# Optimization experiments

Measured on AMD Instinct MI355X. Metric: run time of the kernel, lower is better.

## Reference

```python
import jax, jax.numpy as jnp
import numpy as np

EPS = 1e-5
MAX_DIFF = 0.01


def _conv1d(x, w, b, pad):
    # x: [B,C,L], w: [O,I,K]
    out = jax.lax.conv_general_dilated(x, w, (1,), [(pad, pad)],
                                       dimension_numbers=('NCH', 'OIH', 'NCH'))
    return out + b[None, :, None]


def _maxpool2(x):
    B, C, L = x.shape
    return x.reshape(B, C, L // 2, 2).max(-1)


def setup_inputs() -> dict:
    key = jax.random.key(0)
    ks = jax.random.split(key, 12)
    B, N, F, NF = 64, 750, 8, 250
    inp = {
        'x_sample': jax.random.normal(ks[0], (B, NF), jnp.float32),
        'x_graph': jax.random.normal(ks[1], (B, N, F), jnp.float32),
        'W1': jax.random.normal(ks[2], (NF, 250), jnp.float32) * 0.05,
        'b1': jnp.zeros((250,), jnp.float32),
        'gl': jnp.ones((250,), jnp.float32),
        'bl': jnp.zeros((250,), jnp.float32),
        'Wg': jax.random.normal(ks[3], (F, F), jnp.float32) * 0.3,
        'bg': jnp.zeros((F,), jnp.float32),
        'g1': jnp.ones((1,), jnp.float32),
        'be1': jnp.zeros((1,), jnp.float32),
        'Wc1': jax.random.normal(ks[4], (32, 1, 5), jnp.float32) * 0.3,
        'bc1': jnp.zeros((32,), jnp.float32),
        'gc1': jnp.ones((32,), jnp.float32),
        'bec1': jnp.zeros((32,), jnp.float32),
        'Wc2': jax.random.normal(ks[5], (64, 32, 5), jnp.float32) * 0.08,
        'bc2': jnp.zeros((64,), jnp.float32),
        'gc2': jnp.ones((64,), jnp.float32),
        'bec2': jnp.zeros((64,), jnp.float32),
        'Wc3': jax.random.normal(ks[6], (128, 64, 250), jnp.float32) * 0.008,
        'bc3': jnp.zeros((128,), jnp.float32),
        'Wf': jax.random.normal(ks[7], (128, 64), jnp.float32) * 0.09,
        'bf': jnp.zeros((64,), jnp.float32),
        'gf': jnp.ones((64,), jnp.float32),
        'bef': jnp.zeros((64,), jnp.float32),
        'Wo': jax.random.normal(ks[8], (64, 12), jnp.float32) * 0.12,
        'bo': jnp.zeros((12,), jnp.float32),
    }
    return inp


def reference(x_sample, x_graph, W1, b1, gl, bl, Wg, bg, g1, be1,
              Wc1, bc1, gc1, bec1, Wc2, bc2, gc2, bec2, Wc3, bc3,
              Wf, bf, gf, bef, Wo, bo):
    inv = 1.0 / jnp.sqrt(1.0 + EPS)  # eval-mode BN with mean=0, var=1
    B, N, F = x_graph.shape

    # linear1 -> BN -> ReLU (dropout is identity in eval)
    s = x_sample @ W1 + b1
    s = jax.nn.relu(s * inv * gl + bl)  # [B,250]

    # pairwise-threshold edge construction as dense masked adjacency
    d = x_graph[..., 0]  # [B,N]
    mask = (d[:, :, None] - d[:, None, :]) ** 2 < MAX_DIFF  # symmetric
    eye = jnp.eye(N, dtype=x_graph.dtype)
    A = jnp.where(mask, 1.0, 0.0) * (1.0 - eye) + eye  # + self loops (GCNConv)
    dn = jax.lax.rsqrt(A.sum(-1))  # D^{-1/2}
    An = dn[:, :, None] * A * dn[:, None, :]

    # GCNConv: D^{-1/2}(A+I)D^{-1/2} (X W) + b
    h = jnp.einsum('bij,bjf->bif', An, x_graph @ Wg) + bg
    # BatchNorm2d(1) eval (scalar affine) -> ReLU
    h = jax.nn.relu(h * inv * g1[0] + be1[0])  # [B,N,F]

    g = h.mean(-1)  # [B,N]
    x = jnp.concatenate([s, g], axis=1)[:, None, :]  # [B,1,1000]

    x = _conv1d(x, Wc1, bc1, pad=2)
    x = jax.nn.relu(x * inv * gc1[None, :, None] + bec1[None, :, None])
    x = _maxpool2(x)  # [B,32,500]

    x = _conv1d(x, Wc2, bc2, pad=2)
    x = jax.nn.relu(x * inv * gc2[None, :, None] + bec2[None, :, None])
    x = _maxpool2(x)  # [B,64,250]

    x = _conv1d(x, Wc3, bc3, pad=0)[:, :, 0]  # [B,128]

    x = x @ Wf + bf
    x = jax.nn.relu(x * inv * gf + bef)
    x = x @ Wo + bo
    return jax.nn.log_softmax(x, axis=1)
```

## Files before the change

### kernel.cpp

```cpp
#include <hip/hip_runtime.h>
#include <math.h>

#define NN 750

__device__ __forceinline__ float bn_inv() { return 1.0f / sqrtf(1.0f + 1e-5f); }

__device__ __forceinline__ unsigned encf(float f) {
  unsigned b = __float_as_uint(f);
  return (b & 0x80000000u) ? ~b : (b | 0x80000000u);
}
__device__ __forceinline__ float decf(unsigned u) {
  return __uint_as_float((u & 0x80000000u) ? (u & 0x7fffffffu) : ~u);
}

__global__ __launch_bounds__(256) void k_lin1(
    const float* __restrict__ xs, const float* __restrict__ W1,
    const float* __restrict__ b1, const float* __restrict__ gl,
    const float* __restrict__ bl, float* __restrict__ X0)
{
  int b = blockIdx.x, t = threadIdx.x;
  __shared__ float xsh[250];
  for (int k = t; k < 250; k += 256) xsh[k] = xs[b * 250 + k];
  __syncthreads();
  if (t < 250) {
    float acc = 0.f;
    #pragma unroll 10
    for (int k = 0; k < 250; ++k) acc = fmaf(xsh[k], W1[k * 250 + t], acc);
    float v = (acc + b1[t]) * bn_inv() * gl[t] + bl[t];
    X0[b * 1000 + t] = fmaxf(v, 0.f);
  }
}

__global__ __launch_bounds__(256) void k_gcn_count(
    const float* __restrict__ xg, const float* __restrict__ Wg,
    float* __restrict__ szdn, int* __restrict__ loA, int* __restrict__ hiA,
    float* __restrict__ dnA)
{
  int b = blockIdx.x, c = blockIdx.y, t = threadIdx.x;
  __shared__ unsigned long long kL[NN];
  __shared__ float wgs[64];
  for (int j = t; j < NN; j += 256) {
    float dj = xg[(size_t)(b * NN + j) * 8];
    kL[j] = ((unsigned long long)encf(dj) << 10) | (unsigned)j;
  }
  if (t < 64) wgs[t] = Wg[t];
  __syncthreads();
  if (t >= 250) return;
  int i = c * 250 + t;
  float d = xg[(size_t)(b * NN + i) * 8];
  unsigned long long ki = ((unsigned long long)encf(d) << 10) | (unsigned)i;

  unsigned uf = encf(d - 0.15f);
  unsigned ut = encf(d);
  #pragma unroll 1
  for (int it = 0; it < 33 && (ut - uf) > 1u; ++it) {
    unsigned um = uf + ((ut - uf) >> 1);
    if (d - decf(um) >= 0.1f) uf = um; else ut = um;
  }
  unsigned A1 = ut;
  unsigned vf = encf(d);
  unsigned vt = encf(d + 0.15f);
  #pragma unroll 1
  for (int it = 0; it < 33 && (vt - vf) > 1u; ++it) {
    unsigned um = vf + ((vt - vf) >> 1);
    if (d - decf(um) <= -0.1f) vt = um; else vf = um;
  }
  unsigned B = vt;

  unsigned long long KA = (unsigned long long)A1 << 10;
  unsigned long long KB = (unsigned long long)B << 10;
  int rank = 0, lov = 0, hiv = 0;
  #pragma unroll 6
  for (int j = 0; j < NN; ++j) {
    unsigned long long kj = kL[j];
    rank += (kj < ki);
    lov  += (kj < KA);
    hiv  += (kj < KB);
  }
  int cnt = hiv - lov;
  float dn = 1.0f / sqrtf((float)cnt);

  const float4* xp = (const float4*)(xg + (size_t)(b * NN + i) * 8);
  float4 x0 = xp[0], x1 = xp[1];
  float xv[8] = {x0.x, x0.y, x0.z, x0.w, x1.x, x1.y, x1.z, x1.w};
  float zf[8];
  #pragma unroll
  for (int f = 0; f < 8; ++f) {
    float a = 0.f;
    #pragma unroll
    for (int k = 0; k < 8; ++k) a = fmaf(xv[k], wgs[k * 8 + f], a);
    zf[f] = dn * a;
  }
  float* dst = szdn + ((size_t)b * NN + rank) * 8;
  *(float4*)dst       = make_float4(zf[0], zf[1], zf[2], zf[3]);
  *(float4*)(dst + 4) = make_float4(zf[4], zf[5], zf[6], zf[7]);
  loA[b * NN + i] = lov; hiA[b * NN + i] = hiv; dnA[b * NN + i] = dn;
}

__global__ __launch_bounds__(512) void k_gcn_apply(
    const float* __restrict__ szdn, const int* __restrict__ loA,
    const int* __restrict__ hiA, const float* __restrict__ dnA,
    const float* __restrict__ bgp, const float* __restrict__ g1p,
    const float* __restrict__ be1p, float* __restrict__ X0)
{
  int b = blockIdx.x, t = threadIdx.x;
  __shared__ float P[NN * 8];
  __shared__ float wsum[4 * 8];
  __shared__ float bgs[8];
  if (t < 8) bgs[t] = bgp[t];
  for (int e = t; e < NN * 2; e += 512)
    ((float4*)P)[e] = ((const float4*)(szdn + (size_t)b * NN * 8))[e];
  __syncthreads();

  int lane = t & 63, w = t >> 6;
  bool scanner = (t < 256);
  float e0[8], e01[8], s[8], sc[8];
  if (scanner) {
    int u = t;
    if (u < 250) {
      #pragma unroll
      for (int f = 0; f < 8; ++f) e0[f] = P[(3 * u) * 8 + f];
      #pragma unroll
      for (int f = 0; f < 8; ++f) e01[f] = e0[f] + P[(3 * u + 1) * 8 + f];
      #pragma unroll
      for (int f = 0; f < 8; ++f) s[f] = e01[f] + P[(3 * u + 2) * 8 + f];
    } else {
      #pragma unroll
      for (int f = 0; f < 8; ++f) { e0[f] = 0.f; e01[f] = 0.f; s[f] = 0.f; }
    }
    #pragma unroll
    for (int f = 0; f < 8; ++f) sc[f] = s[f];
    for (int dlt = 1; dlt < 64; dlt <<= 1) {
      float o[8];
      #pragma unroll
      for (int f = 0; f < 8; ++f) o[f] = __shfl_up(sc[f], (unsigned)dlt, 64);
      if (lane >= dlt) {
        #pragma unroll
        for (int f = 0; f < 8; ++f) sc[f] += o[f];
      }
    }
    if (lane == 63) {
      #pragma unroll
      for (int f = 0; f < 8; ++f) wsum[w * 8 + f] = sc[f];
    }
  }
  __syncthreads();
  if (scanner && t < 250) {
    float off[8];
    #pragma unroll
    for (int f = 0; f < 8; ++f) off[f] = 0.f;
    for (int ww = 0; ww < w; ++ww) {
      #pragma unroll
      for (int f = 0; f < 8; ++f) off[f] += wsum[ww * 8 + f];
    }
    int u = t;
    #pragma unroll
    for (int f = 0; f < 8; ++f) {
      float excl = sc[f] - s[f] + off[f];
      P[(3 * u) * 8 + f]     = excl + e0[f];
      P[(3 * u + 1) * 8 + f] = excl + e01[f];
      P[(3 * u + 2) * 8 + f] = excl + s[f];
    }
  }
  __syncthreads();

  float inv = bn_inv(), g1v = g1p[0], be1v = be1p[0];
  for (int nn = t; nn < NN; nn += 512) {
    int lo = loA[b * NN + nn], hi = hiA[b * NN + nn];
    float dn = dnA[b * NN + nn];
    float gsum = 0.f;
    #pragma unroll
    for (int f = 0; f < 8; ++f) {
      float a  = P[(hi - 1) * 8 + f];
      float bb = (lo > 0) ? P[(lo - 1) * 8 + f] : 0.f;
      float h  = dn * (a - bb) + bgs[f];
      float v  = h * inv * g1v + be1v;
      gsum += fmaxf(v, 0.f);
    }
    X0[b * 1000 + 250 + nn] = gsum * 0.125f;
  }
}

__global__ __launch_bounds__(256) void k_conv1(
    const float* __restrict__ X0, const float* __restrict__ Wc1,
    const float* __restrict__ bc1, const float* __restrict__ gc1,
    const float* __restrict__ bec1, float* __restrict__ Y1)
{
  int b = blockIdx.x, p0 = blockIdx.y * 125, tid = threadIdx.x;
  __shared__ float xsh[254];
  __shared__ float w[160], bb[32], gg[32], ee[32];
  for (int i = tid; i < 254; i += 256) {
    int gq = 2 * p0 - 2 + i;
    xsh[i] = (gq >= 0 && gq < 1000) ? X0[b * 1000 + gq] : 0.f;
  }
  for (int i = tid; i < 160; i += 256) w[i] = Wc1[i];
  if (tid < 32) { bb[tid] = bc1[tid]; gg[tid] = gc1[tid]; ee[tid] = bec1[tid]; }
  __syncthreads();
  float inv = bn_inv();
  for (int o = tid; o < 32 * 125; o += 256) {
    int c = o / 125, pl = o % 125;
    int base = 2 * pl;
    float v0 = 0.f, v1 = 0.f;
    #pragma unroll
    for (int k = 0; k < 5; ++k) {
      float wk = w[c * 5 + k];
      v0 = fmaf(xsh[base + k], wk, v0);
      v1 = fmaf(xsh[base + 1 + k], wk, v1);
    }
    float s0 = fmaxf((v0 + bb[c]) * inv * gg[c] + ee[c], 0.f);
    float s1 = fmaxf((v1 + bb[c]) * inv * gg[c] + ee[c], 0.f);
    Y1[((b * 32) + c) * 500 + p0 + pl] = fmaxf(s0, s1);
  }
}

__global__ __launch_bounds__(256) void k_conv2(
    const float* __restrict__ Y1, const float* __restrict__ Wc2,
    const float* __restrict__ bc2, const float* __restrict__ gc2,
    const float* __restrict__ bec2, float* __restrict__ Y2)
{
  int b = blockIdx.x, p0 = blockIdx.y * 52, tid = threadIdx.x;
  __shared__ float xin[32][108];
  __shared__ float ws2[64 * 161];
  for (int e = tid; e < 32 * 108; e += 256) {
    int ci = e / 108, li = e % 108;
    int gq = 2 * p0 - 2 + li;
    xin[ci][li] = (gq >= 0 && gq < 500) ? Y1[((b * 32) + ci) * 500 + gq] : 0.f;
  }
  for (int e = tid; e < 64 * 160; e += 256) {
    int co = e / 160, r = e % 160;
    ws2[co * 161 + r] = Wc2[e];
  }
  __syncthreads();
  int co = tid >> 2, sub = tid & 3;
  int base = sub * 26;
  float acc[26];
  #pragma unroll
  for (int r = 0; r < 26; ++r) acc[r] = 0.f;
  for (int ci = 0; ci < 32; ++ci) {
    float xr[30];
    #pragma unroll
    for (int jj = 0; jj < 30; ++jj) xr[jj] = xin[ci][base + jj];
    #pragma unroll
    for (int k = 0; k < 5; ++k) {
      float wk = ws2[co * 161 + ci * 5 + k];
      #pragma unroll
      for (int r = 0; r < 26; ++r) acc[r] = fmaf(xr[r + k], wk, acc[r]);
    }
  }
  float inv = bn_inv();
  float bc = bc2[co], gc = gc2[co], ec = bec2[co];
  int ps = p0 + sub * 13;
  #pragma unroll
  for (int r = 0; r < 13; ++r) {
    int p = ps + r;
    if (p < 250) {
      float a0 = fmaxf((acc[2 * r] + bc) * inv * gc + ec, 0.f);
      float a1 = fmaxf((acc[2 * r + 1] + bc) * inv * gc + ec, 0.f);
      Y2[((b * 64) + co) * 250 + p] = fmaxf(a0, a1);
    }
  }
}

__global__ __launch_bounds__(256) void k_conv3(
    const float* __restrict__ Y2, const float* __restrict__ Wc3,
    float* __restrict__ C3P, int CP)
{
  int pb = blockIdx.x, tid = threadIdx.x;
  __shared__ float As[64 * 64];
  __shared__ float Bs[64 * 128];
  int bt = tid >> 5, ot = tid & 31;
  int b0 = bt * 8, o0 = ot * 4;
  float4 acc[8];
  #pragma unroll
  for (int r = 0; r < 8; ++r) acc[r] = make_float4(0.f, 0.f, 0.f, 0.f);

  for (int s = 0; s < CP; ++s) {
    int kbase = (pb * CP + s) * 64;
    __syncthreads();
    for (int e = tid; e < 4096; e += 256) {
      int bb = e >> 6, kk = e & 63;
      As[e] = Y2[bb * 16000 + kbase + kk];
    }
    for (int e = tid; e < 8192; e += 256) {
      int o = e >> 6, kk = e & 63;
      float v = Wc3[o * 16000 + kbase + kk];
      Bs[kk * 128 + ((((o >> 2) ^ (kk & 31)) << 2) | (o & 3))] = v;
    }
    __syncthreads();
    for (int ks = 0; ks < 64; ks += 4) {
      float4 av[8];
      #pragma unroll
      for (int r = 0; r < 8; ++r)
        av[r] = *(const float4*)&As[(b0 + r) * 64 + ks];
      float4 bv[4];
      #pragma unroll
      for (int q = 0; q < 4; ++q) {
        int kk = ks + q;
        bv[q] = *(const float4*)&Bs[kk * 128 + ((ot ^ (kk & 31)) << 2)];
      }
      #pragma unroll
      for (int q = 0; q < 4; ++q) {
        #pragma unroll
        for (int r = 0; r < 8; ++r) {
          float a = (q == 0) ? av[r].x : (q == 1) ? av[r].y
                  : (q == 2) ? av[r].z : av[r].w;
          acc[r].x = fmaf(a, bv[q].x, acc[r].x);
          acc[r].y = fmaf(a, bv[q].y, acc[r].y);
          acc[r].z = fmaf(a, bv[q].z, acc[r].z);
          acc[r].w = fmaf(a, bv[q].w, acc[r].w);
        }
      }
    }
  }
  #pragma unroll
  for (int r = 0; r < 8; ++r)
    *(float4*)&C3P[(size_t)pb * 8192 + (b0 + r) * 128 + o0] = acc[r];
}

__global__ __launch_bounds__(256) void k_fc(
    const float* __restrict__ C3P, const float* __restrict__ bc3,
    const float* __restrict__ Wf, const float* __restrict__ bf,
    const float* __restrict__ gf, const float* __restrict__ bef,
    const float* __restrict__ Wo, const float* __restrict__ bo,
    float* __restrict__ out, int NB)
{
  int b = blockIdx.x, t = threadIdx.x;
  __shared__ float zp[8][128];
  __shared__ float z[128];
  __shared__ float fp[4][64];
  __shared__ float f[64];

  int g = t >> 5;
  int o4 = (t & 31) * 4;
  float4 a = make_float4(0.f, 0.f, 0.f, 0.f);
  for (int c = g; c < NB; c += 8) {
    float4 v = *(const float4*)&C3P[(size_t)c * 8192 + b * 128 + o4];
    a.x += v.x; a.y += v.y; a.z += v.z; a.w += v.w;
  }
  *(float4*)&zp[g][o4] = a;
  __syncthreads();
  if (t < 128) {
    float s = bc3[t];
    #pragma unroll
    for (int gg = 0; gg < 8; ++gg) s += zp[gg][t];
    z[t] = s;
  }
  __syncthreads();
  {
    int oo = t & 63, q = t >> 6;
    float acc = 0.f;
    #pragma unroll
    for (int k = 0; k < 32; ++k) {
      int kk = q * 32 + k;
      acc = fmaf(z[kk], Wf[kk * 64 + oo], acc);
    }
    fp[q][oo] = acc;
  }
  __syncthreads();
  if (t < 64) {
    float v = fp[0][t] + fp[1][t] + fp[2][t] + fp[3][t] + bf[t];
    v = v * bn_inv() * gf[t] + bef[t];
    f[t] = fmaxf(v, 0.f);
  }
  __syncthreads();

  if (t < 64) {
    float logit = 0.f;
    if (t < 12) {
      float acc = 0.f;
      #pragma unroll 8
      for (int k = 0; k < 64; ++k) acc = fmaf(f[k], Wo[k * 12 + t], acc);
      logit = acc + bo[t];
    }
    float m = (t < 12) ? logit : -3.4e38f;
    for (int off = 32; off > 0; off >>= 1) m = fmaxf(m, __shfl_xor(m, off));
    float e = (t < 12) ? expf(logit - m) : 0.f;
    float ssum = e;
    for (int off = 32; off > 0; off >>= 1) ssum += __shfl_xor(ssum, off);
    if (t < 12) out[b * 12 + t] = logit - m - logf(ssum);
  }
}

extern "C" void kernel_launch(void* const* d_in, const int* in_sizes, int n_in,
                              void* d_out, int out_size, void* d_ws, size_t ws_size,
                              hipStream_t stream)
{
  const float* xs   = (const float*)d_in[0];
  const float* xg   = (const float*)d_in[1];
  const float* W1   = (const float*)d_in[2];
  const float* b1   = (const float*)d_in[3];
  const float* gl   = (const float*)d_in[4];
  const float* bl   = (const float*)d_in[5];
  const float* Wg   = (const float*)d_in[6];
  const float* bg   = (const float*)d_in[7];
  const float* g1   = (const float*)d_in[8];
  const float* be1  = (const float*)d_in[9];
  const float* Wc1  = (const float*)d_in[10];
  const float* bc1  = (const float*)d_in[11];
  const float* gc1  = (const float*)d_in[12];
  const float* bec1 = (const float*)d_in[13];
  const float* Wc2  = (const float*)d_in[14];
  const float* bc2  = (const float*)d_in[15];
  const float* gc2  = (const float*)d_in[16];
  const float* bec2 = (const float*)d_in[17];
  const float* Wc3  = (const float*)d_in[18];
  const float* bc3  = (const float*)d_in[19];
  const float* Wf   = (const float*)d_in[20];
  const float* bfp  = (const float*)d_in[21];
  const float* gf   = (const float*)d_in[22];
  const float* bef  = (const float*)d_in[23];
  const float* Wo   = (const float*)d_in[24];
  const float* bo   = (const float*)d_in[25];
  float* out = (float*)d_out;

  float* W    = (float*)d_ws;
  float* X0   = W;
  float* Y1   = W + 64000;
  float* Y2   = W + 1088000;
  float* szdn = W + 2112000;
  int*   loA  = (int*)(W + 2496000);
  int*   hiA  = (int*)(W + 2544000);
  float* dnA  = W + 2592000;
  float* C3P  = W + 2640000;

  long availl = (long)(ws_size / 4) - 2640000L;
  const int cand[8] = {250, 125, 50, 25, 10, 5, 2, 1};
  int NB = 1;
  for (int i = 0; i < 8; ++i)
    if ((long)cand[i] * 8192L <= availl) { NB = cand[i]; break; }
  int CP = 250 / NB;

  k_lin1     <<<64, 256, 0, stream>>>(xs, W1, b1, gl, bl, X0);
  k_gcn_count<<<dim3(64, 3), 256, 0, stream>>>(xg, Wg, szdn, loA, hiA, dnA);
  k_gcn_apply<<<64, 512, 0, stream>>>(szdn, loA, hiA, dnA, bg, g1, be1, X0);
  k_conv1    <<<dim3(64, 4), 256, 0, stream>>>(X0, Wc1, bc1, gc1, bec1, Y1);
  k_conv2    <<<dim3(64, 5), 256, 0, stream>>>(Y1, Wc2, bc2, gc2, bec2, Y2);
  k_conv3    <<<NB, 256, 0, stream>>>(Y2, Wc3, C3P, CP);
  k_fc       <<<64, 256, 0, stream>>>(C3P, bc3, Wf, bfp, gf, bef, Wo, bo, out, NB);
}
```

Before: 200.4 us.

## Fuse lin1 into GCN count kernel and conv1 into GCN apply kernel

Result: faster. 194.3 us (-3.0%).

```diff
diff --git a/kernel.cpp b/kernel.cpp
--- a/kernel.cpp
+++ b/kernel.cpp
@@ -13,32 +13,32 @@
   return __uint_as_float((u & 0x80000000u) ? (u & 0x7fffffffu) : ~u);
 }
 
-__global__ __launch_bounds__(256) void k_lin1(
+__global__ __launch_bounds__(256) void k_front(
     const float* __restrict__ xs, const float* __restrict__ W1,
     const float* __restrict__ b1, const float* __restrict__ gl,
-    const float* __restrict__ bl, float* __restrict__ X0)
-{
-  int b = blockIdx.x, t = threadIdx.x;
-  __shared__ float xsh[250];
-  for (int k = t; k < 250; k += 256) xsh[k] = xs[b * 250 + k];
-  __syncthreads();
-  if (t < 250) {
-    float acc = 0.f;
-    #pragma unroll 10
-    for (int k = 0; k < 250; ++k) acc = fmaf(xsh[k], W1[k * 250 + t], acc);
-    float v = (acc + b1[t]) * bn_inv() * gl[t] + bl[t];
-    X0[b * 1000 + t] = fmaxf(v, 0.f);
-  }
-}
-
-__global__ __launch_bounds__(256) void k_gcn_count(
-    const float* __restrict__ xg, const float* __restrict__ Wg,
+    const float* __restrict__ bl, const float* __restrict__ xg,
+    const float* __restrict__ Wg, float* __restrict__ X0s,
     float* __restrict__ szdn, int* __restrict__ loA, int* __restrict__ hiA,
     float* __restrict__ dnA)
 {
-  int b = blockIdx.x, c = blockIdx.y, t = threadIdx.x;
+  int b = blockIdx.x, t = threadIdx.x;
   __shared__ unsigned long long kL[NN];
   __shared__ float wgs[64];
+  __shared__ float xsh[250];
+
+  if (blockIdx.y == 3) {
+    for (int k = t; k < 250; k += 256) xsh[k] = xs[b * 250 + k];
+    __syncthreads();
+    if (t < 250) {
+      float acc = 0.f;
+      #pragma unroll 10
+      for (int k = 0; k < 250; ++k) acc = fmaf(xsh[k], W1[k * 250 + t], acc);
+      float v = (acc + b1[t]) * bn_inv() * gl[t] + bl[t];
+      X0s[b * 250 + t] = fmaxf(v, 0.f);
+    }
+    return;
+  }
+  int c = blockIdx.y;
   for (int j = t; j < NN; j += 256) {
     float dj = xg[(size_t)(b * NN + j) * 8];
     kL[j] = ((unsigned long long)encf(dj) << 10) | (unsigned)j;
@@ -50,16 +50,14 @@
   float d = xg[(size_t)(b * NN + i) * 8];
   unsigned long long ki = ((unsigned long long)encf(d) << 10) | (unsigned)i;
 
-  unsigned uf = encf(d - 0.15f);
-  unsigned ut = encf(d);
+  unsigned uf = encf(d - 0.15f), ut = encf(d);
   #pragma unroll 1
   for (int it = 0; it < 33 && (ut - uf) > 1u; ++it) {
     unsigned um = uf + ((ut - uf) >> 1);
     if (d - decf(um) >= 0.1f) uf = um; else ut = um;
   }
   unsigned A1 = ut;
-  unsigned vf = encf(d);
-  unsigned vt = encf(d + 0.15f);
+  unsigned vf = encf(d), vt = encf(d + 0.15f);
   #pragma unroll 1
   for (int it = 0; it < 33 && (vt - vf) > 1u; ++it) {
     unsigned um = vf + ((vt - vf) >> 1);
@@ -97,17 +95,29 @@
   loA[b * NN + i] = lov; hiA[b * NN + i] = hiv; dnA[b * NN + i] = dn;
 }
 
-__global__ __launch_bounds__(512) void k_gcn_apply(
+__global__ __launch_bounds__(512) void k_apply1(
     const float* __restrict__ szdn, const int* __restrict__ loA,
     const int* __restrict__ hiA, const float* __restrict__ dnA,
     const float* __restrict__ bgp, const float* __restrict__ g1p,
-    const float* __restrict__ be1p, float* __restrict__ X0)
+    const float* __restrict__ be1p, const float* __restrict__ X0s,
+    const float* __restrict__ Wc1, const float* __restrict__ bc1,
+    const float* __restrict__ gc1, const float* __restrict__ bec1,
+    float* __restrict__ Y1)
 {
   int b = blockIdx.x, t = threadIdx.x;
   __shared__ float P[NN * 8];
   __shared__ float wsum[4 * 8];
   __shared__ float bgs[8];
+  __shared__ float xpad[1004];
+  __shared__ float w1s[160], bb1[32], gg1[32], ee1[32];
+
   if (t < 8) bgs[t] = bgp[t];
+  for (int i = t; i < 160; i += 512) w1s[i] = Wc1[i];
+  if (t >= 256 && t < 288) {
+    int q = t - 256; bb1[q] = bc1[q]; gg1[q] = gc1[q]; ee1[q] = bec1[q];
+  }
+  if (t >= 288 && t < 292) xpad[(t - 288) < 2 ? (t - 288) : (1000 + t - 288)] = 0.f;
+  if (t < 250) xpad[2 + t] = X0s[b * 250 + t];
   for (int e = t; e < NN * 2; e += 512)
     ((float4*)P)[e] = ((const float4*)(szdn + (size_t)b * NN * 8))[e];
   __syncthreads();
@@ -177,39 +187,23 @@
       float v  = h * inv * g1v + be1v;
       gsum += fmaxf(v, 0.f);
     }
-    X0[b * 1000 + 250 + nn] = gsum * 0.125f;
-  }
-}
-
-__global__ __launch_bounds__(256) void k_conv1(
-    const float* __restrict__ X0, const float* __restrict__ Wc1,
-    const float* __restrict__ bc1, const float* __restrict__ gc1,
-    const float* __restrict__ bec1, float* __restrict__ Y1)
-{
-  int b = blockIdx.x, p0 = blockIdx.y * 125, tid = threadIdx.x;
-  __shared__ float xsh[254];
-  __shared__ float w[160], bb[32], gg[32], ee[32];
-  for (int i = tid; i < 254; i += 256) {
-    int gq = 2 * p0 - 2 + i;
-    xsh[i] = (gq >= 0 && gq < 1000) ? X0[b * 1000 + gq] : 0.f;
-  }
-  for (int i = tid; i < 160; i += 256) w[i] = Wc1[i];
-  if (tid < 32) { bb[tid] = bc1[tid]; gg[tid] = gc1[tid]; ee[tid] = bec1[tid]; }
-  __syncthreads();
-  float inv = bn_inv();
-  for (int o = tid; o < 32 * 125; o += 256) {
-    int c = o / 125, pl = o % 125;
-    int base = 2 * pl;
+    xpad[2 + 250 + nn] = gsum * 0.125f;
+  }
+  __syncthreads();
+
+  for (int o = t; o < 32 * 500; o += 512) {
+    int c = o / 500, pl = o % 500;
+    int q = 2 * pl;
     float v0 = 0.f, v1 = 0.f;
     #pragma unroll
     for (int k = 0; k < 5; ++k) {
-      float wk = w[c * 5 + k];
-      v0 = fmaf(xsh[base + k], wk, v0);
-      v1 = fmaf(xsh[base + 1 + k], wk, v1);
-    }
-    float s0 = fmaxf((v0 + bb[c]) * inv * gg[c] + ee[c], 0.f);
-    float s1 = fmaxf((v1 + bb[c]) * inv * gg[c] + ee[c], 0.f);
-    Y1[((b * 32) + c) * 500 + p0 + pl] = fmaxf(s0, s1);
+      float wk = w1s[c * 5 + k];
+      v0 = fmaf(xpad[q + k], wk, v0);
+      v1 = fmaf(xpad[q + 1 + k], wk, v1);
+    }
+    float s0 = fmaxf((v0 + bb1[c]) * inv * gg1[c] + ee1[c], 0.f);
+    float s1 = fmaxf((v1 + bb1[c]) * inv * gg1[c] + ee1[c], 0.f);
+    Y1[((b * 32) + c) * 500 + pl] = fmaxf(s0, s1);
   }
 }
 
@@ -263,7 +257,7 @@
 
 __global__ __launch_bounds__(256) void k_conv3(
     const float* __restrict__ Y2, const float* __restrict__ Wc3,
-    float* __restrict__ C3P, int CP)
+    float* __restrict__ C3P, int CP, int NB)
 {
   int pb = blockIdx.x, tid = threadIdx.x;
   __shared__ float As[64 * 64];
@@ -314,7 +308,7 @@
   }
   #pragma unroll
   for (int r = 0; r < 8; ++r)
-    *(float4*)&C3P[(size_t)pb * 8192 + (b0 + r) * 128 + o0] = acc[r];
+    *(float4*)&C3P[((size_t)(b0 + r) * NB + pb) * 128 + o0] = acc[r];
 }
 
 __global__ __launch_bounds__(256) void k_fc(
@@ -334,7 +328,7 @@
   int o4 = (t & 31) * 4;
   float4 a = make_float4(0.f, 0.f, 0.f, 0.f);
   for (int c = g; c < NB; c += 8) {
-    float4 v = *(const float4*)&C3P[(size_t)c * 8192 + b * 128 + o4];
+    float4 v = *(const float4*)&C3P[((size_t)b * NB + c) * 128 + o4];
     a.x += v.x; a.y += v.y; a.z += v.z; a.w += v.w;
   }
   *(float4*)&zp[g][o4] = a;
@@ -414,27 +408,27 @@
   float* out = (float*)d_out;
 
   float* W    = (float*)d_ws;
-  float* X0   = W;
-  float* Y1   = W + 64000;
-  float* Y2   = W + 1088000;
-  float* szdn = W + 2112000;
-  int*   loA  = (int*)(W + 2496000);
-  int*   hiA  = (int*)(W + 2544000);
-  float* dnA  = W + 2592000;
-  float* C3P  = W + 2640000;
-
-  long availl = (long)(ws_size / 4) - 2640000L;
+  float* X0s  = W;
+  float* Y1   = W + 16000;
+  float* Y2   = W + 1040000;
+  float* szdn = W + 2064000;
+  int*   loA  = (int*)(W + 2448000);
+  int*   hiA  = (int*)(W + 2496000);
+  float* dnA  = W + 2544000;
+  float* C3P  = W + 2592000;
+
+  long availl = (long)(ws_size / 4) - 2592000L;
   const int cand[8] = {250, 125, 50, 25, 10, 5, 2, 1};
   int NB = 1;
   for (int i = 0; i < 8; ++i)
     if ((long)cand[i] * 8192L <= availl) { NB = cand[i]; break; }
   int CP = 250 / NB;
 
-  k_lin1     <<<64, 256, 0, stream>>>(xs, W1, b1, gl, bl, X0);
-  k_gcn_count<<<dim3(64, 3), 256, 0, stream>>>(xg, Wg, szdn, loA, hiA, dnA);
-  k_gcn_apply<<<64, 512, 0, stream>>>(szdn, loA, hiA, dnA, bg, g1, be1, X0);
-  k_conv1    <<<dim3(64, 4), 256, 0, stream>>>(X0, Wc1, bc1, gc1, bec1, Y1);
-  k_conv2    <<<dim3(64, 5), 256, 0, stream>>>(Y1, Wc2, bc2, gc2, bec2, Y2);
-  k_conv3    <<<NB, 256, 0, stream>>>(Y2, Wc3, C3P, CP);
-  k_fc       <<<64, 256, 0, stream>>>(C3P, bc3, Wf, bfp, gf, bef, Wo, bo, out, NB);
-}
+  k_front <<<dim3(64, 4), 256, 0, stream>>>(xs, W1, b1, gl, bl, xg, Wg,
+                                            X0s, szdn, loA, hiA, dnA);
+  k_apply1<<<64, 512, 0, stream>>>(szdn, loA, hiA, dnA, bg, g1, be1,
+                                   X0s, Wc1, bc1, gc1, bec1, Y1);
+  k_conv2 <<<dim3(64, 5), 256, 0, stream>>>(Y1, Wc2, bc2, gc2, bec2, Y2);
+  k_conv3 <<<NB, 256, 0, stream>>>(Y2, Wc3, C3P, CP, NB);
+  k_fc    <<<64, 256, 0, stream>>>(C3P, bc3, Wf, bfp, gf, bef, Wo, bo, out, NB);
+}
```
